# Performance work log

Hardware: AMD Instinct MI355X
Metric: run time of the kernel (lower is better)

Reference implementation:

```python
import jax, jax.numpy as jnp
import numpy as np
import math

B, S, HID = 1, 4096, 2048
NH, NKV, HD = 16, 4, 128
SKETCH, TOPK = 640, 2048
EPS = 1e-6


def _dct_orthonormal(rows, cols, rng, sink=4, fsink=8):
    i = np.arange(rows)[:, None]
    j = np.arange(cols)[None, :]
    dct = np.cos(np.pi / cols * (j + 0.5) * i)
    dct[0, :] *= math.sqrt(1.0 / cols)
    dct[1:, :] *= math.sqrt(2.0 / cols)
    signs = rng.integers(0, 2, (1, cols)).astype(np.float64) * 2.0 - 1.0
    m = dct * signs
    m[:, :sink] *= 2.0
    m[:fsink, :] *= 1.5
    return m.astype(np.float32)


def setup_inputs() -> dict:
    key = jax.random.key(0)
    ks = jax.random.split(key, 8)
    rng = np.random.default_rng(0)
    # RoPE tables (b, s, 1, head_dim)
    pos = np.arange(S, dtype=np.float32)
    inv = 1.0 / (10000.0 ** (np.arange(0, HD, 2, dtype=np.float32) / HD))
    ang = pos[:, None] * inv[None, :]              # (S, HD/2)
    emb = np.concatenate([ang, ang], axis=-1)       # (S, HD)
    cos = np.broadcast_to(np.cos(emb)[None, :, None, :], (B, S, 1, HD)).copy()
    sin = np.broadcast_to(np.sin(emb)[None, :, None, :], (B, S, 1, HD)).copy()
    w = 0.02
    return {
        'hidden_states': jax.random.normal(ks[0], (B, S, HID), jnp.float32),
        'wq': jax.random.normal(ks[1], (HID, NH * HD), jnp.float32) * w,
        'wk': jax.random.normal(ks[2], (HID, NKV * HD), jnp.float32) * w,
        'wv': jax.random.normal(ks[3], (HID, NKV * HD), jnp.float32) * w,
        'wo': jax.random.normal(ks[4], (NH * HD, HID), jnp.float32) * w,
        'qn_w': jnp.ones((HD,), jnp.float32),
        'kn_w': jnp.ones((HD,), jnp.float32),
        's_w1': jax.random.normal(ks[5], (HID, 64), jnp.float32) * w,
        's_b1': jnp.zeros((64,), jnp.float32),
        's_w2': jax.random.normal(ks[6], (64, 1), jnp.float32) * w,
        's_b2': jnp.zeros((1,), jnp.float32),
        'sketch_scale': jnp.full((1,), 0.1, jnp.float32),
        'kron_a': jnp.asarray(_dct_orthonormal(20, 128, rng)),
        'kron_b': jnp.asarray(_dct_orthonormal(32, 256, rng)),
        'cos': jnp.asarray(cos),
        'sin': jnp.asarray(sin),
    }


def _rms_norm(x, w):
    var = jnp.mean(jnp.square(x), axis=-1, keepdims=True)
    return x * jax.lax.rsqrt(var + EPS) * w


def _rope(x, cos, sin):
    # x: (b, s, h, d); cos/sin: (b, s, 1, d)
    d2 = x.shape[-1] // 2
    rot = jnp.concatenate([-x[..., d2:], x[..., :d2]], axis=-1)
    return x * cos + rot * sin


def reference(hidden_states, wq, wk, wv, wo, qn_w, kn_w, s_w1, s_b1, s_w2, s_b2,
              sketch_scale, kron_a, kron_b, cos, sin):
    b, s, _ = hidden_states.shape
    # importance scorer with compression pressure bias
    logits = jnp.tanh(hidden_states @ s_w1 + s_b1) @ s_w2 + s_b2   # (b, s, 1)
    if s > SKETCH:
        logits = logits - math.log(s / SKETCH)
    iw = jax.nn.sigmoid(logits)                                    # (b, s, 1)

    q = (hidden_states @ wq).reshape(b, s, NH, HD)
    k = (hidden_states @ wk).reshape(b, s, NKV, HD)
    v = (hidden_states @ wv).reshape(b, s, NKV, HD)
    q = _rms_norm(q, qn_w)
    k = _rms_norm(k, kn_w)

    tk = min(s, TOPK)
    _, idx = jax.lax.top_k(logits[..., 0], tk)                     # (b, tk)
    ix = idx[:, :, None, None]
    k_detail = jnp.take_along_axis(k, ix, axis=1)                  # (b, tk, nkv, d)
    v_detail = jnp.take_along_axis(v, ix, axis=1)
    cos_det = jnp.take_along_axis(cos, ix, axis=1)                 # (b, tk, 1, d)
    sin_det = jnp.take_along_axis(sin, ix, axis=1)

    # Kronecker sketch of importance-weighted K/V over all tokens
    P = jnp.kron(kron_a, kron_b)[:, :s]                            # (640, s)
    kw = k * iw[..., None]
    vw = v * iw[..., None]
    k_sketch = jnp.einsum('bshd,ms->bmhd', kw, P) * sketch_scale
    v_sketch = jnp.einsum('bshd,ms->bmhd', vw, P) * sketch_scale

    q_rope = _rope(q, cos, sin)
    k_detail = _rope(k_detail, cos_det, sin_det)

    k_final = jnp.concatenate([k_detail, k_sketch], axis=1)        # (b, tk+640, nkv, d)
    v_final = jnp.concatenate([v_detail, v_sketch], axis=1)
    rep = NH // NKV
    k_final = jnp.repeat(k_final, rep, axis=2)                     # (b, L, nh, d)
    v_final = jnp.repeat(v_final, rep, axis=2)

    scores = jnp.einsum('bqhd,bkhd->bhqk', q_rope, k_final) / math.sqrt(HD)
    attn = jax.nn.softmax(scores, axis=-1)
    out = jnp.einsum('bhqk,bkhd->bqhd', attn, v_final).reshape(b, s, NH * HD)
    return out @ wo
```

## Files before the change

kernel.cpp:

```cpp
#include <hip/hip_runtime.h>
#include <math.h>

typedef _Float16 f16;
typedef f16 f16x8 __attribute__((ext_vector_type(8)));
typedef float f32x4 __attribute__((ext_vector_type(4)));

#define MFMA16(a,b,c) __builtin_amdgcn_mfma_f32_16x16x32_f16(a,b,c,0,0,0)

static __device__ __forceinline__ f16x8 ld8(const f16* p) { return *(const f16x8*)p; }

static __device__ __forceinline__ float exp2a(float x) {
    float r; asm("v_exp_f32 %0, %1" : "=v"(r) : "v"(x)); return r;
}

#if __has_builtin(__builtin_amdgcn_global_load_lds)
#define GLL16(g, lptr) __builtin_amdgcn_global_load_lds((const __attribute__((address_space(1))) void*)(g), (__attribute__((address_space(3))) void*)(lptr), 16, 0, 0)
#else
#define GLL16(g, lptr) do { *(int4*)(lptr) = *(const int4*)(g); } while (0)
#endif

__global__ __launch_bounds__(256) void k_cvt(const float* __restrict__ in, f16* __restrict__ out) {
    int idx = blockIdx.x * 256 + threadIdx.x;
    int base = idx * 8;
    float4 a = *(const float4*)&in[base];
    float4 b = *(const float4*)&in[base + 4];
    f16x8 v;
    v[0]=(f16)a.x; v[1]=(f16)a.y; v[2]=(f16)a.z; v[3]=(f16)a.w;
    v[4]=(f16)b.x; v[5]=(f16)b.y; v[6]=(f16)b.z; v[7]=(f16)b.w;
    *(f16x8*)&out[base] = v;
}

__global__ __launch_bounds__(256) void k_transpose(const float* __restrict__ in, f16* __restrict__ out,
                                                   int inCols, int rowOff) {
    __shared__ float tile[32][33];
    int tx = threadIdx.x, ty = threadIdx.y;
    int x = blockIdx.x * 32 + tx;
    int y0 = blockIdx.y * 32;
    #pragma unroll
    for (int i = 0; i < 4; ++i)
        tile[ty + i*8][tx] = in[(size_t)(y0 + ty + i*8) * inCols + x];
    __syncthreads();
    #pragma unroll
    for (int i = 0; i < 4; ++i)
        out[(size_t)(rowOff + blockIdx.x*32 + ty + i*8) * 2048 + y0 + tx] = (f16)tile[tx][ty + i*8];
}

__global__ __launch_bounds__(256) void k_mlp(const float* __restrict__ h, const float* __restrict__ w1,
                                             const float* __restrict__ b1, const float* __restrict__ w2,
                                             const float* __restrict__ b2, double* __restrict__ logitsD,
                                             float* __restrict__ iw) {
    __shared__ float hl[4 * 2048];
    __shared__ double tl[4][64];
    int tid = threadIdx.x;
    int s0 = blockIdx.x * 4;
    #pragma unroll
    for (int p = 0; p < 8; ++p) {
        int off = p * 1024 + tid * 4;
        *(float4*)&hl[off] = *(const float4*)&h[(size_t)s0 * 2048 + off];
    }
    __syncthreads();
    int j = tid & 63, r = tid >> 6;
    const float* hr = &hl[r * 2048];
    double acc = 0.0;
    for (int c = 0; c < 2048; ++c) acc += (double)hr[c] * (double)w1[c * 64 + j];
    acc += (double)b1[j];
    tl[r][j] = tanh(acc);
    __syncthreads();
    int lane = tid & 63, rr = tid >> 6;
    double v = tl[rr][lane] * (double)w2[lane];
    for (int o = 32; o > 0; o >>= 1) v += __shfl_down(v, o);
    if (lane == 0) {
        double lg = v + (double)b2[0] - 1.8562979903656263;
        logitsD[s0 + rr] = lg;
        iw[s0 + rr] = (float)(1.0 / (1.0 + exp(-lg)));
    }
}

__global__ __launch_bounds__(1024) void k_topk(const double* __restrict__ logitsD, int* __restrict__ sel) {
    __shared__ unsigned long long keys[4096];
    __shared__ unsigned int hist[2048];
    __shared__ unsigned int bcast[2];
    __shared__ unsigned int cA, cB;
    int tid = threadIdx.x;
    for (int i = tid; i < 4096; i += 1024) {
        unsigned long long u = (unsigned long long)__double_as_longlong(logitsD[i]);
        keys[i] = (u >> 63) ? ~u : (u | 0x8000000000000000ull);
    }
    if (tid == 0) { cA = 0; cB = 0; }
    unsigned long long Tpart = 0;
    unsigned int need = 2048;
    #pragma unroll 1
    for (int lvl = 0; lvl < 6; ++lvl) {
        int shift = (lvl < 5) ? (53 - 11*lvl) : 0;
        int width = (lvl < 5) ? 11 : 9;
        unsigned int nb = 1u << width;
        int hiShift = shift + width;
        for (int i = tid; i < (int)nb; i += 1024) hist[i] = 0;
        __syncthreads();
        for (int i = tid; i < 4096; i += 1024) {
            unsigned long long k = keys[i];
            bool cand = (lvl == 0) || ((k >> hiShift) == (Tpart >> hiShift));
            if (cand) atomicAdd(&hist[(unsigned int)(k >> shift) & (nb - 1u)], 1u);
        }
        __syncthreads();
        if (tid < 64) {
            int chunk = (int)nb >> 6;
            int base = (int)nb - (tid + 1) * chunk;
            unsigned int sum = 0;
            for (int j = 0; j < chunk; ++j) sum += hist[base + j];
            unsigned int pre = sum;
            #pragma unroll
            for (int o = 1; o < 64; o <<= 1) {
                unsigned int t = __shfl_up(pre, o);
                if (tid >= o) pre += t;
            }
            unsigned int preEx = pre - sum;
            if (preEx < need && need <= pre) {
                unsigned int cum = preEx;
                for (int j = chunk - 1; j >= 0; --j) {
                    unsigned int c = hist[base + j];
                    if (cum + c >= need) { bcast[0] = (unsigned int)(base + j); bcast[1] = need - cum; break; }
                    cum += c;
                }
            }
        }
        __syncthreads();
        Tpart |= ((unsigned long long)bcast[0]) << shift;
        need = bcast[1];
        __syncthreads();
    }
    unsigned int G = 2048 - need;
    for (int i = tid; i < 4096; i += 1024) {
        unsigned long long k = keys[i];
        if (k > Tpart) { unsigned int p = atomicAdd(&cA, 1u); sel[p] = i; }
        else if (k == Tpart) { unsigned int q = atomicAdd(&cB, 1u); if (q < need) sel[G + q] = i; }
    }
}

__global__ __launch_bounds__(256) void k_gemm(const f16* __restrict__ A, const f16* __restrict__ Bt,
                                              float* __restrict__ C, int M, int N, int K) {
    __shared__ f16 As[128 * 32];
    __shared__ f16 Bs[128 * 32];
    int tid = threadIdx.x;
    int w = tid >> 6, l = tid & 63, lr = l & 15, lg = l >> 4;
    int wr = w >> 1, wc = w & 1;
    int row0 = blockIdx.y * 128, col0 = blockIdx.x * 128;
    f32x4 zero = {0.f, 0.f, 0.f, 0.f};
    f32x4 acc[4][4];
    #pragma unroll
    for (int m = 0; m < 4; ++m)
        #pragma unroll
        for (int n = 0; n < 4; ++n) acc[m][n] = zero;
    for (int k0 = 0; k0 < K; k0 += 32) {
        #pragma unroll
        for (int p = 0; p < 2; ++p) {
            int id = p * 256 + tid;
            int r = id >> 2, c8 = (id & 3) * 8;
            GLL16(&A[(size_t)(row0 + r) * K + k0 + c8], &As[id * 8]);
            GLL16(&Bt[(size_t)(col0 + r) * K + k0 + c8], &Bs[id * 8]);
        }
        __syncthreads();
        f16x8 a[4], b[4];
        #pragma unroll
        for (int m = 0; m < 4; ++m) a[m] = ld8(&As[(wr*64 + m*16 + lr) * 32 + lg*8]);
        #pragma unroll
        for (int n = 0; n < 4; ++n) b[n] = ld8(&Bs[(wc*64 + n*16 + lr) * 32 + lg*8]);
        #pragma unroll
        for (int m = 0; m < 4; ++m)
            #pragma unroll
            for (int n = 0; n < 4; ++n)
                acc[m][n] = MFMA16(a[m], b[n], acc[m][n]);
        __syncthreads();
    }
    #pragma unroll
    for (int m = 0; m < 4; ++m)
        #pragma unroll
        for (int n = 0; n < 4; ++n)
            #pragma unroll
            for (int i = 0; i < 4; ++i)
                C[(size_t)(row0 + wr*64 + m*16 + lg*4 + i) * N + col0 + wc*64 + n*16 + lr] = acc[m][n][i];
}

__global__ __launch_bounds__(256) void k_normq(const float* __restrict__ qkv, const float* __restrict__ qnw,
                                               const float* __restrict__ cosb, const float* __restrict__ sinb,
                                               f16* __restrict__ qr) {
    int s = blockIdx.x;
    int tid = threadIdx.x;
    int h = tid >> 4, ln = tid & 15, d0 = ln * 8;
    const float* src = &qkv[(size_t)s * 3072 + h * 128 + d0];
    float4 a = *(const float4*)src, b = *(const float4*)(src + 4);
    float x[8] = {a.x,a.y,a.z,a.w,b.x,b.y,b.z,b.w};
    float ss = 0;
    #pragma unroll
    for (int j = 0; j < 8; ++j) ss += x[j]*x[j];
    ss += __shfl_xor(ss,1); ss += __shfl_xor(ss,2); ss += __shfl_xor(ss,4); ss += __shfl_xor(ss,8);
    float rn = rsqrtf(ss * (1.0f/128.0f) + 1e-6f);
    float xn[8];
    #pragma unroll
    for (int j = 0; j < 8; ++j) xn[j] = x[j] * rn * qnw[d0 + j];
    const float scl = 0.088388347648318447f * 1.4426950408889634f;
    f16x8 o;
    #pragma unroll
    for (int j = 0; j < 8; ++j) {
        float pr = __shfl_xor(xn[j], 8);
        float rot = (ln < 8) ? -pr : pr;
        int d = d0 + j;
        o[j] = (f16)((xn[j]*cosb[s*128 + d] + rot*sinb[s*128 + d]) * scl);
    }
    *(f16x8*)&qr[(size_t)s * 2048 + h * 128 + d0] = o;
}

__global__ __launch_bounds__(64) void k_normk(const float* __restrict__ qkv, const float* __restrict__ knw,
                                              float* __restrict__ kn) {
    int s = blockIdx.x;
    int tid = threadIdx.x;
    int h = tid >> 4, ln = tid & 15, d0 = ln * 8;
    const float* src = &qkv[(size_t)s * 3072 + 2048 + h * 128 + d0];
    float4 a = *(const float4*)src, b = *(const float4*)(src + 4);
    float x[8] = {a.x,a.y,a.z,a.w,b.x,b.y,b.z,b.w};
    float ss = 0;
    #pragma unroll
    for (int j = 0; j < 8; ++j) ss += x[j]*x[j];
    ss += __shfl_xor(ss,1); ss += __shfl_xor(ss,2); ss += __shfl_xor(ss,4); ss += __shfl_xor(ss,8);
    float rn = rsqrtf(ss * (1.0f/128.0f) + 1e-6f);
    float o[8];
    #pragma unroll
    for (int j = 0; j < 8; ++j) o[j] = x[j] * rn * knw[d0 + j];
    float* dst = &kn[(size_t)s*512 + h*128 + d0];
    *(float4*)dst = make_float4(o[0],o[1],o[2],o[3]);
    *(float4*)(dst+4) = make_float4(o[4],o[5],o[6],o[7]);
}

__global__ __launch_bounds__(128) void k_gather(const int* __restrict__ sel, const float* __restrict__ kn,
                                                const float* __restrict__ qkv, const float* __restrict__ cosb,
                                                const float* __restrict__ sinb, f16* __restrict__ Kf,
                                                f16* __restrict__ VfT) {
    int j = blockIdx.x;
    int s = sel[j];
    int t = threadIdx.x;
    float c = cosb[s*128 + t], sn = sinb[s*128 + t];
    #pragma unroll
    for (int h = 0; h < 4; ++h) {
        float x  = kn[(size_t)s*512 + h*128 + t];
        float pr = kn[(size_t)s*512 + h*128 + (t ^ 64)];
        float rot = (t < 64) ? -pr : pr;
        Kf[(size_t)(h*2688 + j) * 128 + t] = (f16)(x*c + rot*sn);
        float v = qkv[(size_t)s*3072 + 2560 + h*128 + t];
        VfT[(size_t)h*128*2688 + (size_t)t*2688 + j] = (f16)v;
    }
}

__global__ __launch_bounds__(256) void k_sketch1(const float* __restrict__ kn, const float* __restrict__ qkv,
                                                 const float* __restrict__ iw, const float* __restrict__ kronb,
                                                 float* __restrict__ T) {
    int mb = blockIdx.x & 31, sa = blockIdx.x >> 5;
    int which = blockIdx.y;
    int c0 = threadIdx.x * 2;
    float a0 = 0, a1 = 0;
    for (int sb = 0; sb < 256; ++sb) {
        int s = sa * 256 + sb;
        float wgt = kronb[mb * 256 + sb] * iw[s];
        const float* src = which ? &qkv[(size_t)s*3072 + 2560] : &kn[(size_t)s*512];
        a0 += wgt * src[c0];
        a1 += wgt * src[c0 + 1];
    }
    float* dst = &T[(size_t)((which*32 + mb)*16 + sa) * 512 + c0];
    dst[0] = a0; dst[1] = a1;
}

__global__ __launch_bounds__(256) void k_sketch2(const float* __restrict__ T, const float* __restrict__ krona,
                                                 const float* __restrict__ sscale, f16* __restrict__ Kf,
                                                 f16* __restrict__ VfT) {
    int m = blockIdx.x;
    int which = blockIdx.y;
    int ma = m >> 5, mb = m & 31;
    int c0 = threadIdx.x * 2;
    float sc = sscale[0];
    float a0 = 0, a1 = 0;
    #pragma unroll
    for (int sa = 0; sa < 16; ++sa) {
        float ka = krona[ma * 128 + sa];
        const float* t = &T[(size_t)((which*32 + mb)*16 + sa) * 512 + c0];
        a0 += ka * t[0];
        a1 += ka * t[1];
    }
    a0 *= sc; a1 *= sc;
    int key = 2048 + m;
    int h0 = c0 >> 7, d = c0 & 127;
    if (which == 0) {
        Kf[(size_t)(h0*2688 + key)*128 + d]     = (f16)a0;
        Kf[(size_t)(h0*2688 + key)*128 + d + 1] = (f16)a1;
    } else {
        VfT[(size_t)h0*128*2688 + (size_t)d*2688 + key]       = (f16)a0;
        VfT[(size_t)h0*128*2688 + (size_t)(d+1)*2688 + key]   = (f16)a1;
    }
}

__global__ __launch_bounds__(256, 2) void k_attn(const f16* __restrict__ qr, const f16* __restrict__ Kf,
                                                 const f16* __restrict__ VfT, f16* __restrict__ out16) {
    __shared__ f16 KT[2][64 * 128];
    __shared__ f16 VT[2][128 * 64];
    __shared__ f16 P[4][32 * 64];
    int qt = blockIdx.x, h = blockIdx.y;
    int kvh = h >> 2;
    int tid = threadIdx.x;
    int w = tid >> 6, l = tid & 63, lr = l & 15, lg = l >> 4;
    int q0 = qt * 128 + w * 32;
    const char* Kb = (const char*)(Kf + (size_t)kvh * 2688 * 128);
    const char* Vb = (const char*)(VfT + (size_t)kvh * 128 * 2688);
    char* Pw = (char*)&P[w][0];

    int koff[4], voff[2];
    #pragma unroll
    for (int c = 0; c < 4; ++c) koff[c] = (c*64 + lg*16) ^ ((lr & 7) << 5);
    #pragma unroll
    for (int kw = 0; kw < 2; ++kw) voff[kw] = (kw*64 + lg*16) ^ ((lr & 7) << 4);
    int psw = (lr & 7) << 4;

    int L0 = tid * 16;

    f16x8 aq[2][4];
    #pragma unroll
    for (int hh = 0; hh < 2; ++hh)
        #pragma unroll
        for (int c = 0; c < 4; ++c)
            aq[hh][c] = ld8(&qr[(size_t)(q0 + hh*16 + lr) * 2048 + h*128 + c*32 + lg*8]);

    f32x4 zero = {0.f,0.f,0.f,0.f};
    f32x4 o0[8], o1[8];
    #pragma unroll
    for (int f = 0; f < 8; ++f) { o0[f] = zero; o1[f] = zero; }
    float m0[4], m1[4], ls0[4], ls1[4];
    #pragma unroll
    for (int i = 0; i < 4; ++i) { m0[i] = -1e30f; m1[i] = -1e30f; ls0[i] = 0.f; ls1[i] = 0.f; }

    #define STAGE(buf, kt)  do {                                                          \
        _Pragma("unroll")                                                                  \
        for (int i_ = 0; i_ < 4; ++i_) {                                                   \
            int L = L0 + i_*4096;                                                          \
            int krow = L >> 8, kbc = L & 255;                                              \
            GLL16(Kb + (size_t)((kt) + krow)*256 + (kbc ^ ((krow & 7) << 5)),              \
                  (char*)&KT[buf][0] + L);                                                 \
            int vd = L >> 7, vbc = L & 127;                                                \
            GLL16(Vb + (size_t)vd*5376 + (size_t)(kt)*2 + (vbc ^ ((vd & 7) << 4)),         \
                  (char*)&VT[buf][0] + L);                                                 \
        }                                                                                  \
    } while (0)

    STAGE(0, 0);
    asm volatile("s_waitcnt vmcnt(0)" ::: "memory");
    __syncthreads();

    for (int t = 0; t < 42; ++t) {
        int cur = t & 1;
        if (t < 41) STAGE(cur ^ 1, (t + 1) * 64);
        const char* Kc = (const char*)&KT[cur][0];
        const char* Vc = (const char*)&VT[cur][0];

        f32x4 s0[4], s1[4];
        #pragma unroll
        for (int tt = 0; tt < 4; ++tt) { s0[tt] = zero; s1[tt] = zero; }
        __builtin_amdgcn_s_setprio(1);
        #pragma unroll
        for (int tt = 0; tt < 4; ++tt) {
            #pragma unroll
            for (int c = 0; c < 4; ++c) {
                f16x8 kb = ld8((const f16*)(Kc + (tt*16 + lr)*256 + koff[c]));
                s0[tt] = MFMA16(aq[0][c], kb, s0[tt]);
                s1[tt] = MFMA16(aq[1][c], kb, s1[tt]);
            }
        }
        __builtin_amdgcn_s_setprio(0);

        float tm0[4], tm1[4];
        #pragma unroll
        for (int i = 0; i < 4; ++i) {
            float a = fmaxf(fmaxf(s0[0][i], s0[1][i]), fmaxf(s0[2][i], s0[3][i]));
            a = fmaxf(a, __shfl_xor(a, 1)); a = fmaxf(a, __shfl_xor(a, 2));
            a = fmaxf(a, __shfl_xor(a, 4)); a = fmaxf(a, __shfl_xor(a, 8));
            tm0[i] = a;
            float b = fmaxf(fmaxf(s1[0][i], s1[1][i]), fmaxf(s1[2][i], s1[3][i]));
            b = fmaxf(b, __shfl_xor(b, 1)); b = fmaxf(b, __shfl_xor(b, 2));
            b = fmaxf(b, __shfl_xor(b, 4)); b = fmaxf(b, __shfl_xor(b, 8));
            tm1[i] = b;
        }
        bool need = false;
        #pragma unroll
        for (int i = 0; i < 4; ++i) need = need || (tm0[i] > m0[i]+8.f) || (tm1[i] > m1[i]+8.f);
        if (__any(need)) {
            f32x4 cf0, cf1;
            #pragma unroll
            for (int i = 0; i < 4; ++i) {
                float mn0 = fmaxf(m0[i], tm0[i]);
                cf0[i] = exp2a(m0[i] - mn0); m0[i] = mn0; ls0[i] *= cf0[i];
                float mn1 = fmaxf(m1[i], tm1[i]);
                cf1[i] = exp2a(m1[i] - mn1); m1[i] = mn1; ls1[i] *= cf1[i];
            }
            #pragma unroll
            for (int f = 0; f < 8; ++f) { o0[f] *= cf0; o1[f] *= cf1; }
        }
        #pragma unroll
        for (int tt = 0; tt < 4; ++tt)
            #pragma unroll
            for (int i = 0; i < 4; ++i) {
                int r0 = lg*4 + i;
                float p0 = exp2a(s0[tt][i] - m0[i]);
                ls0[i] += p0;
                *(f16*)(Pw + ((r0*128 + (tt*16+lr)*2) ^ ((r0 & 7) << 4))) = (f16)p0;
                int r1 = 16 + r0;
                float p1 = exp2a(s1[tt][i] - m1[i]);
                ls1[i] += p1;
                *(f16*)(Pw + ((r1*128 + (tt*16+lr)*2) ^ ((r1 & 7) << 4))) = (f16)p1;
            }
        asm volatile("s_waitcnt lgkmcnt(0)" ::: "memory");
        __builtin_amdgcn_sched_barrier(0);

        __builtin_amdgcn_s_setprio(1);
        #pragma unroll
        for (int kw = 0; kw < 2; ++kw) {
            f16x8 pa0 = *(const f16x8*)(Pw + ((lr*128 + kw*64 + lg*16) ^ psw));
            f16x8 pa1 = *(const f16x8*)(Pw + (((16+lr)*128 + kw*64 + lg*16) ^ psw));
            #pragma unroll
            for (int f = 0; f < 8; ++f) {
                f16x8 vb = ld8((const f16*)(Vc + (f*16 + lr)*128 + voff[kw]));
                o0[f] = MFMA16(pa0, vb, o0[f]);
                o1[f] = MFMA16(pa1, vb, o1[f]);
            }
        }
        __builtin_amdgcn_s_setprio(0);
        asm volatile("s_waitcnt vmcnt(0)" ::: "memory");
        __syncthreads();
    }

    #pragma unroll
    for (int i = 0; i < 4; ++i) {
        float a = ls0[i];
        a += __shfl_xor(a, 1); a += __shfl_xor(a, 2); a += __shfl_xor(a, 4); a += __shfl_xor(a, 8);
        float inv0 = 1.0f / a;
        float b = ls1[i];
        b += __shfl_xor(b, 1); b += __shfl_xor(b, 2); b += __shfl_xor(b, 4); b += __shfl_xor(b, 8);
        float inv1 = 1.0f / b;
        #pragma unroll
        for (int f = 0; f < 8; ++f) {
            out16[(size_t)(q0 + lg*4 + i) * 2048 + h*128 + f*16 + lr]      = (f16)(o0[f][i] * inv0);
            out16[(size_t)(q0 + 16 + lg*4 + i) * 2048 + h*128 + f*16 + lr] = (f16)(o1[f][i] * inv1);
        }
    }
    #undef STAGE
}

extern "C" void kernel_launch(void* const* d_in, const int* in_sizes, int n_in,
                              void* d_out, int out_size, void* d_ws, size_t ws_size,
                              hipStream_t stream) {
    const float* h     = (const float*)d_in[0];
    const float* wq    = (const float*)d_in[1];
    const float* wk    = (const float*)d_in[2];
    const float* wv    = (const float*)d_in[3];
    const float* wo    = (const float*)d_in[4];
    const float* qnw   = (const float*)d_in[5];
    const float* knw   = (const float*)d_in[6];
    const float* sw1   = (const float*)d_in[7];
    const float* sb1   = (const float*)d_in[8];
    const float* sw2   = (const float*)d_in[9];
    const float* sb2   = (const float*)d_in[10];
    const float* sscal = (const float*)d_in[11];
    const float* ka    = (const float*)d_in[12];
    const float* kb    = (const float*)d_in[13];
    const float* cosb  = (const float*)d_in[14];
    const float* sinb  = (const float*)d_in[15];
    float* outp = (float*)d_out;

    char* ws = (char*)d_ws;
    size_t off = 0;
    f16*    h16    = (f16*)(ws + off);   off += (size_t)4096*2048*2;
    f16*    wqkvt  = (f16*)(ws + off);   off += (size_t)3072*2048*2;
    f16*    wot    = (f16*)(ws + off);   off += (size_t)2048*2048*2;
    float*  qkvraw = (float*)(ws + off); off += (size_t)4096*3072*4;
    f16*    qr     = (f16*)(ws + off);   off += (size_t)4096*2048*2;
    float*  kn     = (float*)(ws + off); off += (size_t)4096*512*4;
    f16*    attn16 = (f16*)(ws + off);   off += (size_t)4096*2048*2;
    float*  T      = (float*)(ws + off); off += (size_t)2*32*16*512*4;
    f16*    Kf     = (f16*)(ws + off);   off += (size_t)4*2688*128*2;
    f16*    VfT    = (f16*)(ws + off);   off += (size_t)4*128*2688*2;
    double* logitsD= (double*)(ws + off);off += (size_t)4096*8;
    float*  iw     = (float*)(ws + off); off += (size_t)4096*4;
    int*    sel    = (int*)(ws + off);   off += (size_t)2048*4;

    k_cvt<<<4096, 256, 0, stream>>>(h, h16);
    k_transpose<<<dim3(64,64), dim3(32,8), 0, stream>>>(wq, wqkvt, 2048, 0);
    k_transpose<<<dim3(16,64), dim3(32,8), 0, stream>>>(wk, wqkvt, 512, 2048);
    k_transpose<<<dim3(16,64), dim3(32,8), 0, stream>>>(wv, wqkvt, 512, 2560);
    k_transpose<<<dim3(64,64), dim3(32,8), 0, stream>>>(wo, wot, 2048, 0);
    k_mlp<<<1024, 256, 0, stream>>>(h, sw1, sb1, sw2, sb2, logitsD, iw);
    k_topk<<<1, 1024, 0, stream>>>(logitsD, sel);
    k_gemm<<<dim3(24,32), 256, 0, stream>>>(h16, wqkvt, qkvraw, 4096, 3072, 2048);
    k_normq<<<4096, 256, 0, stream>>>(qkvraw, qnw, cosb, sinb, qr);
    k_normk<<<4096, 64, 0, stream>>>(qkvraw, knw, kn);
    k_gather<<<2048, 128, 0, stream>>>(sel, kn, qkvraw, cosb, sinb, Kf, VfT);
    k_sketch1<<<dim3(512,2), 256, 0, stream>>>(kn, qkvraw, iw, kb, T);
    k_sketch2<<<dim3(640,2), 256, 0, stream>>>(T, ka, sscal, Kf, VfT);
    k_attn<<<dim3(32,16), 256, 0, stream>>>(qr, Kf, VfT, attn16);
    k_gemm<<<dim3(16,32), 256, 0, stream>>>(attn16, wot, outp, 4096, 2048, 2048);
}
```

Before: 461.3 us.

## Fuse small prep kernels and defer row-max shuffles in attention

Moves the fp32-to-fp16 conversion of hidden states into the MLP scoring kernel, which already holds those rows in shared memory. It also merges the three QKV weight transposes into one launch and merges the Q and K norm kernels into one 320-thread kernel. In attention, the cross-lane max shuffles now run only when a rescale is needed; the threshold check uses each lane's local max instead. This removes several launches and one read of the hidden states, at the cost of a more complex MLP kernel and a 320-thread block shape.

Result: faster. 432.2 us (-6.3%).

```diff
diff --git a/kernel.cpp b/kernel.cpp
--- a/kernel.cpp
+++ b/kernel.cpp
@@ -19,36 +19,10 @@
 #define GLL16(g, lptr) do { *(int4*)(lptr) = *(const int4*)(g); } while (0)
 #endif
 
-__global__ __launch_bounds__(256) void k_cvt(const float* __restrict__ in, f16* __restrict__ out) {
-    int idx = blockIdx.x * 256 + threadIdx.x;
-    int base = idx * 8;
-    float4 a = *(const float4*)&in[base];
-    float4 b = *(const float4*)&in[base + 4];
-    f16x8 v;
-    v[0]=(f16)a.x; v[1]=(f16)a.y; v[2]=(f16)a.z; v[3]=(f16)a.w;
-    v[4]=(f16)b.x; v[5]=(f16)b.y; v[6]=(f16)b.z; v[7]=(f16)b.w;
-    *(f16x8*)&out[base] = v;
-}
-
-__global__ __launch_bounds__(256) void k_transpose(const float* __restrict__ in, f16* __restrict__ out,
-                                                   int inCols, int rowOff) {
-    __shared__ float tile[32][33];
-    int tx = threadIdx.x, ty = threadIdx.y;
-    int x = blockIdx.x * 32 + tx;
-    int y0 = blockIdx.y * 32;
-    #pragma unroll
-    for (int i = 0; i < 4; ++i)
-        tile[ty + i*8][tx] = in[(size_t)(y0 + ty + i*8) * inCols + x];
-    __syncthreads();
-    #pragma unroll
-    for (int i = 0; i < 4; ++i)
-        out[(size_t)(rowOff + blockIdx.x*32 + ty + i*8) * 2048 + y0 + tx] = (f16)tile[tx][ty + i*8];
-}
-
 __global__ __launch_bounds__(256) void k_mlp(const float* __restrict__ h, const float* __restrict__ w1,
                                              const float* __restrict__ b1, const float* __restrict__ w2,
                                              const float* __restrict__ b2, double* __restrict__ logitsD,
-                                             float* __restrict__ iw) {
+                                             float* __restrict__ iw, f16* __restrict__ h16) {
     __shared__ float hl[4 * 2048];
     __shared__ double tl[4][64];
     int tid = threadIdx.x;
@@ -59,6 +33,14 @@
         *(float4*)&hl[off] = *(const float4*)&h[(size_t)s0 * 2048 + off];
     }
     __syncthreads();
+    #pragma unroll
+    for (int p = 0; p < 4; ++p) {
+        int off = p * 2048 + tid * 8;
+        f16x8 v;
+        #pragma unroll
+        for (int j = 0; j < 8; ++j) v[j] = (f16)hl[off + j];
+        *(f16x8*)&h16[(size_t)s0 * 2048 + off] = v;
+    }
     int j = tid & 63, r = tid >> 6;
     const float* hr = &hl[r * 2048];
     double acc = 0.0;
@@ -76,6 +58,41 @@
     }
 }
 
+__global__ __launch_bounds__(256) void k_transpose_qkv(const float* __restrict__ wq, const float* __restrict__ wk,
+                                                       const float* __restrict__ wv, f16* __restrict__ out) {
+    __shared__ float tile[32][33];
+    int bx = blockIdx.x;
+    const float* in; int inCols, colBase, rowOff;
+    if (bx < 64)      { in = wq; inCols = 2048; colBase = bx * 32;        rowOff = colBase; }
+    else if (bx < 80) { in = wk; inCols = 512;  colBase = (bx - 64) * 32; rowOff = 2048 + colBase; }
+    else              { in = wv; inCols = 512;  colBase = (bx - 80) * 32; rowOff = 2560 + colBase; }
+    int tx = threadIdx.x, ty = threadIdx.y;
+    int x = colBase + tx;
+    int y0 = blockIdx.y * 32;
+    #pragma unroll
+    for (int i = 0; i < 4; ++i)
+        tile[ty + i*8][tx] = in[(size_t)(y0 + ty + i*8) * inCols + x];
+    __syncthreads();
+    #pragma unroll
+    for (int i = 0; i < 4; ++i)
+        out[(size_t)(rowOff + ty + i*8) * 2048 + y0 + tx] = (f16)tile[tx][ty + i*8];
+}
+
+__global__ __launch_bounds__(256) void k_transpose(const float* __restrict__ in, f16* __restrict__ out,
+                                                   int inCols, int rowOff) {
+    __shared__ float tile[32][33];
+    int tx = threadIdx.x, ty = threadIdx.y;
+    int x = blockIdx.x * 32 + tx;
+    int y0 = blockIdx.y * 32;
+    #pragma unroll
+    for (int i = 0; i < 4; ++i)
+        tile[ty + i*8][tx] = in[(size_t)(y0 + ty + i*8) * inCols + x];
+    __syncthreads();
+    #pragma unroll
+    for (int i = 0; i < 4; ++i)
+        out[(size_t)(rowOff + blockIdx.x*32 + ty + i*8) * 2048 + y0 + tx] = (f16)tile[tx][ty + i*8];
+}
+
 __global__ __launch_bounds__(1024) void k_topk(const double* __restrict__ logitsD, int* __restrict__ sel) {
     __shared__ unsigned long long keys[4096];
     __shared__ unsigned int hist[2048];
@@ -181,54 +198,53 @@
                 C[(size_t)(row0 + wr*64 + m*16 + lg*4 + i) * N + col0 + wc*64 + n*16 + lr] = acc[m][n][i];
 }
 
-__global__ __launch_bounds__(256) void k_normq(const float* __restrict__ qkv, const float* __restrict__ qnw,
-                                               const float* __restrict__ cosb, const float* __restrict__ sinb,
-                                               f16* __restrict__ qr) {
-    int s = blockIdx.x;
-    int tid = threadIdx.x;
-    int h = tid >> 4, ln = tid & 15, d0 = ln * 8;
-    const float* src = &qkv[(size_t)s * 3072 + h * 128 + d0];
-    float4 a = *(const float4*)src, b = *(const float4*)(src + 4);
-    float x[8] = {a.x,a.y,a.z,a.w,b.x,b.y,b.z,b.w};
-    float ss = 0;
-    #pragma unroll
-    for (int j = 0; j < 8; ++j) ss += x[j]*x[j];
-    ss += __shfl_xor(ss,1); ss += __shfl_xor(ss,2); ss += __shfl_xor(ss,4); ss += __shfl_xor(ss,8);
-    float rn = rsqrtf(ss * (1.0f/128.0f) + 1e-6f);
-    float xn[8];
-    #pragma unroll
-    for (int j = 0; j < 8; ++j) xn[j] = x[j] * rn * qnw[d0 + j];
-    const float scl = 0.088388347648318447f * 1.4426950408889634f;
-    f16x8 o;
-    #pragma unroll
-    for (int j = 0; j < 8; ++j) {
-        float pr = __shfl_xor(xn[j], 8);
-        float rot = (ln < 8) ? -pr : pr;
-        int d = d0 + j;
-        o[j] = (f16)((xn[j]*cosb[s*128 + d] + rot*sinb[s*128 + d]) * scl);
-    }
-    *(f16x8*)&qr[(size_t)s * 2048 + h * 128 + d0] = o;
-}
-
-__global__ __launch_bounds__(64) void k_normk(const float* __restrict__ qkv, const float* __restrict__ knw,
+__global__ __launch_bounds__(320) void k_norm(const float* __restrict__ qkv, const float* __restrict__ qnw,
+                                              const float* __restrict__ knw, const float* __restrict__ cosb,
+                                              const float* __restrict__ sinb, f16* __restrict__ qr,
                                               float* __restrict__ kn) {
     int s = blockIdx.x;
     int tid = threadIdx.x;
-    int h = tid >> 4, ln = tid & 15, d0 = ln * 8;
-    const float* src = &qkv[(size_t)s * 3072 + 2048 + h * 128 + d0];
-    float4 a = *(const float4*)src, b = *(const float4*)(src + 4);
-    float x[8] = {a.x,a.y,a.z,a.w,b.x,b.y,b.z,b.w};
-    float ss = 0;
-    #pragma unroll
-    for (int j = 0; j < 8; ++j) ss += x[j]*x[j];
-    ss += __shfl_xor(ss,1); ss += __shfl_xor(ss,2); ss += __shfl_xor(ss,4); ss += __shfl_xor(ss,8);
-    float rn = rsqrtf(ss * (1.0f/128.0f) + 1e-6f);
-    float o[8];
-    #pragma unroll
-    for (int j = 0; j < 8; ++j) o[j] = x[j] * rn * knw[d0 + j];
-    float* dst = &kn[(size_t)s*512 + h*128 + d0];
-    *(float4*)dst = make_float4(o[0],o[1],o[2],o[3]);
-    *(float4*)(dst+4) = make_float4(o[4],o[5],o[6],o[7]);
+    if (tid < 256) {
+        int h = tid >> 4, ln = tid & 15, d0 = ln * 8;
+        const float* src = &qkv[(size_t)s * 3072 + h * 128 + d0];
+        float4 a = *(const float4*)src, b = *(const float4*)(src + 4);
+        float x[8] = {a.x,a.y,a.z,a.w,b.x,b.y,b.z,b.w};
+        float ss = 0;
+        #pragma unroll
+        for (int j = 0; j < 8; ++j) ss += x[j]*x[j];
+        ss += __shfl_xor(ss,1); ss += __shfl_xor(ss,2); ss += __shfl_xor(ss,4); ss += __shfl_xor(ss,8);
+        float rn = rsqrtf(ss * (1.0f/128.0f) + 1e-6f);
+        float xn[8];
+        #pragma unroll
+        for (int j = 0; j < 8; ++j) xn[j] = x[j] * rn * qnw[d0 + j];
+        const float scl = 0.088388347648318447f * 1.4426950408889634f;
+        f16x8 o;
+        #pragma unroll
+        for (int j = 0; j < 8; ++j) {
+            float pr = __shfl_xor(xn[j], 8);
+            float rot = (ln < 8) ? -pr : pr;
+            int d = d0 + j;
+            o[j] = (f16)((xn[j]*cosb[s*128 + d] + rot*sinb[s*128 + d]) * scl);
+        }
+        *(f16x8*)&qr[(size_t)s * 2048 + h * 128 + d0] = o;
+    } else {
+        int t2 = tid - 256;
+        int h = t2 >> 4, ln = t2 & 15, d0 = ln * 8;
+        const float* src = &qkv[(size_t)s * 3072 + 2048 + h * 128 + d0];
+        float4 a = *(const float4*)src, b = *(const float4*)(src + 4);
+        float x[8] = {a.x,a.y,a.z,a.w,b.x,b.y,b.z,b.w};
+        float ss = 0;
+        #pragma unroll
+        for (int j = 0; j < 8; ++j) ss += x[j]*x[j];
+        ss += __shfl_xor(ss,1); ss += __shfl_xor(ss,2); ss += __shfl_xor(ss,4); ss += __shfl_xor(ss,8);
+        float rn = rsqrtf(ss * (1.0f/128.0f) + 1e-6f);
+        float o[8];
+        #pragma unroll
+        for (int j = 0; j < 8; ++j) o[j] = x[j] * rn * knw[d0 + j];
+        float* dst = &kn[(size_t)s*512 + h*128 + d0];
+        *(float4*)dst = make_float4(o[0],o[1],o[2],o[3]);
+        *(float4*)(dst+4) = make_float4(o[4],o[5],o[6],o[7]);
+    }
 }
 
 __global__ __launch_bounds__(128) void k_gather(const int* __restrict__ sel, const float* __restrict__ kn,
@@ -372,28 +388,27 @@
         }
         __builtin_amdgcn_s_setprio(0);
 
-        float tm0[4], tm1[4];
+        float tl0[4], tl1[4];
+        bool need = false;
         #pragma unroll
         for (int i = 0; i < 4; ++i) {
-            float a = fmaxf(fmaxf(s0[0][i], s0[1][i]), fmaxf(s0[2][i], s0[3][i]));
-            a = fmaxf(a, __shfl_xor(a, 1)); a = fmaxf(a, __shfl_xor(a, 2));
-            a = fmaxf(a, __shfl_xor(a, 4)); a = fmaxf(a, __shfl_xor(a, 8));
-            tm0[i] = a;
-            float b = fmaxf(fmaxf(s1[0][i], s1[1][i]), fmaxf(s1[2][i], s1[3][i]));
-            b = fmaxf(b, __shfl_xor(b, 1)); b = fmaxf(b, __shfl_xor(b, 2));
-            b = fmaxf(b, __shfl_xor(b, 4)); b = fmaxf(b, __shfl_xor(b, 8));
-            tm1[i] = b;
-        }
-        bool need = false;
-        #pragma unroll
-        for (int i = 0; i < 4; ++i) need = need || (tm0[i] > m0[i]+8.f) || (tm1[i] > m1[i]+8.f);
+            tl0[i] = fmaxf(fmaxf(s0[0][i], s0[1][i]), fmaxf(s0[2][i], s0[3][i]));
+            tl1[i] = fmaxf(fmaxf(s1[0][i], s1[1][i]), fmaxf(s1[2][i], s1[3][i]));
+            need = need || (tl0[i] > m0[i]+8.f) || (tl1[i] > m1[i]+8.f);
+        }
         if (__any(need)) {
             f32x4 cf0, cf1;
             #pragma unroll
             for (int i = 0; i < 4; ++i) {
-                float mn0 = fmaxf(m0[i], tm0[i]);
+                float a = tl0[i];
+                a = fmaxf(a, __shfl_xor(a, 1)); a = fmaxf(a, __shfl_xor(a, 2));
+                a = fmaxf(a, __shfl_xor(a, 4)); a = fmaxf(a, __shfl_xor(a, 8));
+                float mn0 = fmaxf(m0[i], a);
                 cf0[i] = exp2a(m0[i] - mn0); m0[i] = mn0; ls0[i] *= cf0[i];
-                float mn1 = fmaxf(m1[i], tm1[i]);
+                float b = tl1[i];
+                b = fmaxf(b, __shfl_xor(b, 1)); b = fmaxf(b, __shfl_xor(b, 2));
+                b = fmaxf(b, __shfl_xor(b, 4)); b = fmaxf(b, __shfl_xor(b, 8));
+                float mn1 = fmaxf(m1[i], b);
                 cf1[i] = exp2a(m1[i] - mn1); m1[i] = mn1; ls1[i] *= cf1[i];
             }
             #pragma unroll
@@ -486,16 +501,12 @@
     float*  iw     = (float*)(ws + off); off += (size_t)4096*4;
     int*    sel    = (int*)(ws + off);   off += (size_t)2048*4;
 
-    k_cvt<<<4096, 256, 0, stream>>>(h, h16);
-    k_transpose<<<dim3(64,64), dim3(32,8), 0, stream>>>(wq, wqkvt, 2048, 0);
-    k_transpose<<<dim3(16,64), dim3(32,8), 0, stream>>>(wk, wqkvt, 512, 2048);
-    k_transpose<<<dim3(16,64), dim3(32,8), 0, stream>>>(wv, wqkvt, 512, 2560);
+    k_mlp<<<1024, 256, 0, stream>>>(h, sw1, sb1, sw2, sb2, logitsD, iw, h16);
+    k_transpose_qkv<<<dim3(96,64), dim3(32,8), 0, stream>>>(wq, wk, wv, wqkvt);
     k_transpose<<<dim3(64,64), dim3(32,8), 0, stream>>>(wo, wot, 2048, 0);
-    k_mlp<<<1024, 256, 0, stream>>>(h, sw1, sb1, sw2, sb2, logitsD, iw);
     k_topk<<<1, 1024, 0, stream>>>(logitsD, sel);
     k_gemm<<<dim3(24,32), 256, 0, stream>>>(h16, wqkvt, qkvraw, 4096, 3072, 2048);
-    k_normq<<<4096, 256, 0, stream>>>(qkvraw, qnw, cosb, sinb, qr);
-    k_normk<<<4096, 64, 0, stream>>>(qkvraw, knw, kn);
+    k_norm<<<4096, 320, 0, stream>>>(qkvraw, qnw, knw, cosb, sinb, qr, kn);
     k_gather<<<2048, 128, 0, stream>>>(sel, kn, qkvraw, cosb, sinb, Kf, VfT);
     k_sketch1<<<dim3(512,2), 256, 0, stream>>>(kn, qkvraw, iw, kb, T);
     k_sketch2<<<dim3(640,2), 256, 0, stream>>>(T, ka, sscal, Kf, VfT);
```
